# Kernel optimization log

Measured on AMD Instinct MI355X. Metric: run time of the kernel, lower is better.

Reference implementation:

```python
import jax, jax.numpy as jnp
import numpy as np

UP_RATIO = 4

def _gen_grid():
    # gen_grid(4): num_x=num_y=2, linspace(-0.2,0.2,2), meshgrid 'ij'
    g = jnp.array([-0.2, 0.2], dtype=jnp.float32)
    x, y = jnp.meshgrid(g, g, indexing='ij')
    return jnp.stack([x, y], axis=-1).reshape(-1, 2)  # [4, 2]

def setup_inputs() -> dict:
    key = jax.random.key(0)
    ks = jax.random.split(key, 12)
    B, C, N = 8, 128, 1024
    Cin = C + 2            # 130, channels after grid concat
    Cq = Cin // 4          # 32
    sc = 0.05
    f32 = jnp.float32
    inputs = jax.random.normal(ks[0], (B, C, N), f32)
    WF = jax.random.normal(ks[1], (Cq, Cin), f32) * sc
    bF = jnp.zeros((Cq,), f32)
    WG = jax.random.normal(ks[2], (Cq, Cin), f32) * sc
    bG = jnp.zeros((Cq,), f32)
    WH = jax.random.normal(ks[3], (Cin, Cin), f32) * sc
    bH = jnp.zeros((Cin,), f32)
    gamma = jnp.float32(0.5)  # torch inits to 0; nonzero so attention path is exercised
    W1 = jax.random.normal(ks[4], (256, Cin), f32) * sc
    b1 = jnp.zeros((256,), f32)
    W2 = jax.random.normal(ks[5], (128, 256), f32) * sc
    b2 = jnp.zeros((128,), f32)
    return dict(inputs=inputs, WF=WF, bF=bF, WG=WG, bG=bG, WH=WH, bH=bH,
                gamma=gamma, W1=W1, b1=b1, W2=W2, b2=b2)

def _conv1x1(W, b, x):
    # Conv1d(kernel_size=1): x [B,C,M] -> [B,O,M]
    return jnp.einsum('oc,bcm->bom', W, x) + b[:, None]

def reference(inputs, WF, bF, WG, bG, WH, bH, gamma, W1, b1, W2, b2):
    B, C, N = inputs.shape
    up = UP_RATIO
    grid = jnp.repeat(_gen_grid(), N, axis=0)          # [up*N, 2], block-repeated per grid row
    net = jnp.transpose(inputs, (0, 2, 1))             # [B, N, C]
    net = jnp.tile(net, (1, up, 1))                    # [B, up*N, C]
    net = jnp.concatenate([net, jnp.broadcast_to(grid, (B, up * N, 2))], axis=2)
    net = jnp.transpose(net, (0, 2, 1))                # [B, C+2, M]
    # attention_unit
    f = jax.nn.relu(_conv1x1(WF, bF, net))             # [B, 32, M]
    g = jax.nn.relu(_conv1x1(WG, bG, net))             # [B, 32, M]
    h = jax.nn.relu(_conv1x1(WH, bH, net))             # [B, 130, M]
    s = jnp.einsum('bcm,bcn->bmn', g, f)               # g^T f : [B, M, M]
    beta = jax.nn.softmax(s, axis=2)
    o = jnp.einsum('bck,bkm->bcm', h, beta)            # h @ beta
    x = gamma * o + net
    x = jax.nn.relu(_conv1x1(W1, b1, x))               # [B, 256, M]
    x = jax.nn.relu(_conv1x1(W2, b2, x))               # [B, 128, M]
    return x
```

## Files before the change

### kernel.cpp

```cpp
#include <hip/hip_runtime.h>
#include <hip/hip_bf16.h>
#include <math.h>

#define BB    8
#define CC    128
#define NN    1024
#define MM    4096
#define CIN   130
#define NROWS 194
#define MPAD  72
#define CIN_P 160
#define OPAD  208


typedef __attribute__((ext_vector_type(8))) short   bf16x8;
typedef __attribute__((ext_vector_type(4))) float   f32x4;
typedef __attribute__((ext_vector_type(8))) unsigned short u16x8;
typedef __attribute__((ext_vector_type(4))) unsigned short u16x4;

static __device__ __forceinline__ unsigned short f2bf(float f) {
    union { float f; unsigned u; } v; v.f = f;
    unsigned r = v.u + 0x7FFFu + ((v.u >> 16) & 1u);
    return (unsigned short)(r >> 16);
}
static __device__ __forceinline__ float bf2f(unsigned short s) {
    union { unsigned u; float f; } v; v.u = ((unsigned)s) << 16;
    return v.f;
}

#define MFMA16(a, b, c) __builtin_amdgcn_mfma_f32_16x16x32_bf16((a), (b), (c), 0, 0, 0)

__global__ __launch_bounds__(256) void prep_kernel(
    const float* __restrict__ W1, const float* __restrict__ W2,
    const float* __restrict__ WF, const float* __restrict__ WG,
    const float* __restrict__ WH, const float* __restrict__ bFp,
    const float* __restrict__ bGp, const float* __restrict__ bHp,
    unsigned short* __restrict__ W1b, unsigned short* __restrict__ W2b,
    unsigned short* __restrict__ Wfgh, float* __restrict__ bfgh,
    float* __restrict__ Lsum)
{
    int i = blockIdx.x * 256 + threadIdx.x;
    if (i < 40960) {
        int o = i / CIN_P, c = i - o * CIN_P;
        W1b[i] = (c < CIN) ? f2bf(W1[o * CIN + c]) : (unsigned short)0;
    } else if (i < 73728) {
        int j = i - 40960;
        W2b[j] = f2bf(W2[j]);
    } else if (i < 107008) {
        int j = i - 73728;
        int o = j / CIN_P, c = j - o * CIN_P;
        float w = 0.f;
        if (c < CIN) {
            if (o < 32)         w = WF[o * CIN + c];
            else if (o < 64)    w = WG[(o - 32) * CIN + c];
            else if (o < NROWS) w = WH[(o - 64) * CIN + c];
        }
        Wfgh[j] = f2bf(w);
    } else if (i < 107216) {
        int o = i - 107008;
        float bv = 0.f;
        if (o < 32)         bv = bFp[o];
        else if (o < 64)    bv = bGp[o - 32];
        else if (o < NROWS) bv = bHp[o - 64];
        bfgh[o] = bv;
    } else if (i < 139984) {
        Lsum[i - 107216] = 0.f;
    }
}

__global__ __launch_bounds__(256) void transpose_kernel(
    const float* __restrict__ inp, unsigned short* __restrict__ net_t)
{
    const int b  = blockIdx.y;
    const int n0 = blockIdx.x * 32;
    const int t  = threadIdx.x;

    __shared__ float tile[CC][33];

    for (int idx = t; idx < CC * 32; idx += 256) {
        int c = idx >> 5, n = idx & 31;
        tile[c][n] = inp[((size_t)b * CC + c) * NN + n0 + n];
    }
    __syncthreads();

    const int n = t >> 3, grp = t & 7;
    #pragma unroll
    for (int q = 0; q < 4; ++q) {
        const int m = q * NN + n0 + n;
        const float gx = (q >> 1) ? 0.2f : -0.2f;
        const float gy = (q & 1)  ? 0.2f : -0.2f;
        for (int j = grp; j < 20; j += 8) {
            const int c0 = j * 8;
            u16x8 pk;
            #pragma unroll
            for (int i = 0; i < 8; ++i) {
                int c = c0 + i;
                float v = (c < CC) ? tile[c][n]
                        : (c == CC) ? gx : (c == CC + 1) ? gy : 0.f;
                pk[i] = f2bf(v);
            }
            *(u16x8*)&net_t[((size_t)b * MM + m) * CIN_P + c0] = pk;
        }
    }
}

__global__ __launch_bounds__(256) void proj_kernel(
    const unsigned short* __restrict__ Wfgh, const float* __restrict__ bfgh,
    const unsigned short* __restrict__ net_t,
    unsigned short* __restrict__ f_t, unsigned short* __restrict__ g_t,
    unsigned short* __restrict__ h)
{
    const int lane = threadIdx.x & 63, w = threadIdx.x >> 6;
    const int l15 = lane & 15, lg = lane >> 4;
    const int mg = blockIdx.x * 64 + w * 16 + l15;
    const int b = mg >> 12, m = mg & (MM - 1);

    bf16x8 nf[5];
    #pragma unroll
    for (int ks = 0; ks < 5; ++ks)
        nf[ks] = *(const bf16x8*)&net_t[(size_t)mg * CIN_P + ks * 32 + lg * 8];

    const f32x4 zero = {0.f, 0.f, 0.f, 0.f};

    #pragma unroll
    for (int ot = 0; ot < 13; ++ot) {
        f32x4 acc = zero;
        #pragma unroll
        for (int ks = 0; ks < 5; ++ks) {
            bf16x8 aW = *(const bf16x8*)&Wfgh[(size_t)(ot * 16 + l15) * CIN_P + ks * 32 + lg * 8];
            acc = MFMA16(aW, nf[ks], acc);
        }
        const int o0 = ot * 16 + lg * 4;
        float v[4];
        #pragma unroll
        for (int r = 0; r < 4; ++r) v[r] = fmaxf(acc[r] + bfgh[o0 + r], 0.f);

        if (ot < 2) {
            u16x4 pk;
            #pragma unroll
            for (int r = 0; r < 4; ++r) pk[r] = f2bf(v[r]);
            *(u16x4*)&f_t[(size_t)mg * 32 + o0] = pk;
        } else if (ot < 4) {
            u16x4 pk;
            #pragma unroll
            for (int r = 0; r < 4; ++r) pk[r] = f2bf(v[r]);
            *(u16x4*)&g_t[(size_t)mg * 32 + (o0 - 32)] = pk;
        } else {
            #pragma unroll
            for (int r = 0; r < 4; ++r) {
                int o = o0 + r;
                if (o < NROWS)
                    h[((size_t)b * CIN + (o - 64)) * MM + m] = f2bf(v[r]);
            }
        }
    }
}

__global__ __launch_bounds__(256) void rowstats_kernel(
    const unsigned short* __restrict__ f_t, const unsigned short* __restrict__ g_t,
    float* __restrict__ Lsum)
{
    const int b  = blockIdx.y;
    const int k0 = blockIdx.x * 64;
    const int m0 = blockIdx.z * 1024;
    const int lane = threadIdx.x & 63, w = threadIdx.x >> 6;
    const int l15 = lane & 15, lg = lane >> 4;

    const bf16x8 aG = *(const bf16x8*)&g_t[((size_t)b * MM + k0 + w * 16 + l15) * 32 + lg * 8];
    const f32x4 zero = {0.f, 0.f, 0.f, 0.f};
    f32x4 sum = zero;

    for (int mc = m0; mc < m0 + 1024; mc += 64) {
        #pragma unroll
        for (int mt = 0; mt < 4; ++mt) {
            bf16x8 fB = *(const bf16x8*)&f_t[((size_t)b * MM + mc + mt * 16 + l15) * 32 + lg * 8];
            f32x4 s = MFMA16(aG, fB, zero);
            #pragma unroll
            for (int r = 0; r < 4; ++r) sum[r] += __expf(s[r] - 4.0f);
        }
    }

    #pragma unroll
    for (int d = 1; d < 16; d <<= 1) {
        #pragma unroll
        for (int r = 0; r < 4; ++r) sum[r] += __shfl_xor(sum[r], d);
    }
    if (l15 == 0) {
        #pragma unroll
        for (int r = 0; r < 4; ++r)
            atomicAdd(&Lsum[b * MM + k0 + w * 16 + lg * 4 + r], sum[r]);
    }
}

__global__ __launch_bounds__(256) void attn_kernel(
    const unsigned short* __restrict__ f_t, const unsigned short* __restrict__ g_t,
    const unsigned short* __restrict__ h,   const float* __restrict__ Lsum,
    float* __restrict__ P)
{
    const int b  = blockIdx.y;
    const int m0 = blockIdx.x * 64;
    const int kz = blockIdx.z;
    const int tid = threadIdx.x;
    const int lane = tid & 63, w = tid >> 6;
    const int l15 = lane & 15, lg = lane >> 4;

    __shared__ unsigned short Hs[144 * MPAD];
    __shared__ unsigned short Et[64 * MPAD];

    const f32x4 zero = {0.f, 0.f, 0.f, 0.f};

    bf16x8 fF[4];
    #pragma unroll
    for (int mt = 0; mt < 4; ++mt)
        fF[mt] = *(const bf16x8*)&f_t[((size_t)b * MM + m0 + mt * 16 + l15) * 32 + lg * 8];

    f32x4 acc[9];
    #pragma unroll
    for (int ct = 0; ct < 9; ++ct) acc[ct] = zero;

    const int kbeg = kz * (MM / 2), kend = kbeg + (MM / 2);
    for (int kc = kbeg; kc < kend; kc += 64) {
        bf16x8 hst[5];
        #pragma unroll
        for (int u = 0; u < 5; ++u) {
            int idx = tid + u * 256;
            int c = idx >> 3, seg = idx & 7;
            bf16x8 v = {0,0,0,0,0,0,0,0};
            if (idx < 1152 && c < CIN)
                v = *(const bf16x8*)&h[((size_t)b * CIN + c) * MM + kc + seg * 8];
            hst[u] = v;
        }

        bf16x8 aG = *(const bf16x8*)&g_t[((size_t)b * MM + kc + w * 16 + l15) * 32 + lg * 8];
        float rinv[4];
        #pragma unroll
        for (int r = 0; r < 4; ++r)
            rinv[r] = 1.0f / Lsum[b * MM + kc + w * 16 + lg * 4 + r];

        f32x4 s[4];
        #pragma unroll
        for (int mt = 0; mt < 4; ++mt)
            s[mt] = MFMA16(aG, fF[mt], zero);

        __syncthreads();

        #pragma unroll
        for (int mt = 0; mt < 4; ++mt) {
            u16x4 pk;
            #pragma unroll
            for (int r = 0; r < 4; ++r)
                pk[r] = f2bf(__expf(s[mt][r] - 4.0f) * rinv[r]);
            *(u16x4*)&Et[(size_t)(mt * 16 + l15) * MPAD + w * 16 + lg * 4] = pk;
        }
        #pragma unroll
        for (int u = 0; u < 5; ++u) {
            int idx = tid + u * 256;
            int c = idx >> 3, seg = idx & 7;
            if (idx < 1152)
                *(bf16x8*)&Hs[(size_t)c * MPAD + seg * 8] = hst[u];
        }
        __syncthreads();

        bf16x8 eB[2];
        #pragma unroll
        for (int ks = 0; ks < 2; ++ks)
            eB[ks] = *(const bf16x8*)&Et[(size_t)(w * 16 + l15) * MPAD + ks * 32 + lg * 8];
        #pragma unroll
        for (int ct = 0; ct < 9; ++ct) {
            #pragma unroll
            for (int ks = 0; ks < 2; ++ks) {
                bf16x8 aH = *(const bf16x8*)&Hs[(size_t)(ct * 16 + l15) * MPAD + ks * 32 + lg * 8];
                acc[ct] = MFMA16(aH, eB[ks], acc[ct]);
            }
        }
    }

    const int m = m0 + w * 16 + l15;
    #pragma unroll
    for (int ct = 0; ct < 9; ++ct) {
        #pragma unroll
        for (int r = 0; r < 4; ++r) {
            const int c = ct * 16 + lg * 4 + r;
            if (c < CIN)
                P[((size_t)(kz * BB + b) * CIN + c) * MM + m] = acc[ct][r];
        }
    }
}

__global__ __launch_bounds__(256) void combine_kernel(
    const float* __restrict__ P, const unsigned short* __restrict__ net_t,
    const float* __restrict__ gamma_p, unsigned short* __restrict__ x_t)
{
    const int b = blockIdx.y;
    const int moff = threadIdx.x & 63, cg = threadIdx.x >> 6;
    const int m = blockIdx.x * 64 + moff;
    const float gam = gamma_p[0];

    #pragma unroll
    for (int j = 0; j < 5; ++j) {
        const int c0 = cg * 40 + j * 8;
        u16x8 net8 = *(const u16x8*)&net_t[((size_t)b * MM + m) * CIN_P + c0];
        u16x8 pk;
        #pragma unroll
        for (int i = 0; i < 8; ++i) {
            const int c = c0 + i;
            if (c < CIN) {
                float p0 = P[((size_t)(0 * BB + b) * CIN + c) * MM + m];
                float p1 = P[((size_t)(1 * BB + b) * CIN + c) * MM + m];
                pk[i] = f2bf(gam * (p0 + p1) + bf2f(net8[i]));
            } else {
                pk[i] = 0;
            }
        }
        *(u16x8*)&x_t[((size_t)b * MM + m) * CIN_P + c0] = pk;
    }
}

template <int KS, int OT, bool OUTF32>
__global__ __launch_bounds__(256) void conv_mfma_kernel(
    const unsigned short* __restrict__ Wb, const float* __restrict__ bias,
    const unsigned short* __restrict__ in_t,
    unsigned short* __restrict__ out_bf, float* __restrict__ out_f32)
{
    const int CINP = KS * 32;
    const int lane = threadIdx.x & 63, w = threadIdx.x >> 6;
    const int l15 = lane & 15, lg = lane >> 4;
    const int m = blockIdx.x * 64 + w * 16 + l15;

    bf16x8 bFr[KS];
    #pragma unroll
    for (int ks = 0; ks < KS; ++ks)
        bFr[ks] = *(const bf16x8*)&in_t[(size_t)m * CINP + ks * 32 + lg * 8];

    const f32x4 zero = {0.f, 0.f, 0.f, 0.f};

    #pragma unroll
    for (int ot = 0; ot < OT; ++ot) {
        f32x4 acc = zero;
        #pragma unroll
        for (int ks = 0; ks < KS; ++ks) {
            bf16x8 aW = *(const bf16x8*)&Wb[(size_t)(ot * 16 + l15) * CINP + ks * 32 + lg * 8];
            acc = MFMA16(aW, bFr[ks], acc);
        }
        const int obase = ot * 16 + lg * 4;
        if (OUTF32) {
            const int bb = m >> 12, mm = m & (MM - 1);
            #pragma unroll
            for (int r = 0; r < 4; ++r)
                out_f32[((size_t)bb * (OT * 16) + obase + r) * MM + mm] =
                    fmaxf(acc[r] + bias[obase + r], 0.f);
        } else {
            u16x4 pk;
            #pragma unroll
            for (int r = 0; r < 4; ++r)
                pk[r] = f2bf(fmaxf(acc[r] + bias[obase + r], 0.f));
            *(u16x4*)&out_bf[(size_t)m * (OT * 16) + obase] = pk;
        }
    }
}

extern "C" void kernel_launch(void* const* d_in, const int* in_sizes, int n_in,
                              void* d_out, int out_size, void* d_ws, size_t ws_size,
                              hipStream_t stream)
{
    const float* inp   = (const float*)d_in[0];
    const float* WF    = (const float*)d_in[1];
    const float* bF    = (const float*)d_in[2];
    const float* WG    = (const float*)d_in[3];
    const float* bG    = (const float*)d_in[4];
    const float* WH    = (const float*)d_in[5];
    const float* bH    = (const float*)d_in[6];
    const float* gamma = (const float*)d_in[7];
    const float* W1    = (const float*)d_in[8];
    const float* b1    = (const float*)d_in[9];
    const float* W2    = (const float*)d_in[10];
    const float* b2    = (const float*)d_in[11];
    float* out = (float*)d_out;

    char* p = (char*)d_ws;
    auto alloc = [&](size_t bytes) { char* q = p; p += (bytes + 255) & ~(size_t)255; return q; };
    unsigned short* net_t = (unsigned short*)alloc((size_t)BB * MM * CIN_P * 2);
    unsigned short* f_t   = (unsigned short*)alloc((size_t)BB * MM * 32 * 2);
    unsigned short* g_t   = (unsigned short*)alloc((size_t)BB * MM * 32 * 2);
    unsigned short* h     = (unsigned short*)alloc((size_t)BB * CIN * MM * 2);
    float*          Lsum  = (float*)alloc((size_t)BB * MM * 4);
    unsigned short* x_t   = (unsigned short*)alloc((size_t)BB * MM * CIN_P * 2);
    float*          P     = (float*)alloc((size_t)2 * BB * CIN * MM * 4);
    unsigned short* x1_t  = (unsigned short*)P;
    unsigned short* W1b   = (unsigned short*)alloc((size_t)256 * CIN_P * 2);
    unsigned short* W2b   = (unsigned short*)alloc((size_t)128 * 256 * 2);
    unsigned short* Wfgh  = (unsigned short*)alloc((size_t)OPAD * CIN_P * 2);
    float*          bfgh  = (float*)alloc((size_t)OPAD * 4);

    prep_kernel<<<547, 256, 0, stream>>>(W1, W2, WF, WG, WH, bF, bG, bH,
                                         W1b, W2b, Wfgh, bfgh, Lsum);

    transpose_kernel<<<dim3(NN / 32, BB), 256, 0, stream>>>(inp, net_t);

    proj_kernel<<<dim3(BB * MM / 64), 256, 0, stream>>>(
        Wfgh, bfgh, net_t, f_t, g_t, h);

    rowstats_kernel<<<dim3(MM / 64, BB, 4), 256, 0, stream>>>(f_t, g_t, Lsum);

    attn_kernel<<<dim3(MM / 64, BB, 2), 256, 0, stream>>>(f_t, g_t, h, Lsum, P);

    combine_kernel<<<dim3(MM / 64, BB), 256, 0, stream>>>(P, net_t, gamma, x_t);

    conv_mfma_kernel<5, 16, false><<<dim3(BB * MM / 64), 256, 0, stream>>>(
        W1b, b1, x_t, x1_t, nullptr);

    conv_mfma_kernel<8, 8, true><<<dim3(BB * MM / 64), 256, 0, stream>>>(
        W2b, b2, x1_t, nullptr, out);
}
```

Baseline: 298.3 us.

## Restructure attention kernel into per-wave 32-column tiles with direct global H loads

The attention kernel now processes 128 output columns per block, with each wave owning 32 columns and computing its own 64-key score tile into a private, XOR-swizzled LDS region. The shared H staging and the block-wide __syncthreads are removed: H fragments are read directly from global memory and reused across two column tiles. The reciprocal is switched to a hardware rcp. The aim is to drop block barriers and LDS traffic for H, at the cost of redundant global H reads per wave, recomputation of exp per wave, and halving the grid size.

After: 372.4 us. 1.25x slower.

```diff
diff --git a/kernel.cpp b/kernel.cpp
--- a/kernel.cpp
+++ b/kernel.cpp
@@ -8,7 +8,6 @@
 #define MM    4096
 #define CIN   130
 #define NROWS 194
-#define MPAD  72
 #define CIN_P 160
 #define OPAD  208
 
@@ -198,91 +197,91 @@
     float* __restrict__ P)
 {
     const int b  = blockIdx.y;
-    const int m0 = blockIdx.x * 64;
+    const int m0 = blockIdx.x * 128;
     const int kz = blockIdx.z;
     const int tid = threadIdx.x;
     const int lane = tid & 63, w = tid >> 6;
     const int l15 = lane & 15, lg = lane >> 4;
 
-    __shared__ unsigned short Hs[144 * MPAD];
-    __shared__ unsigned short Et[64 * MPAD];
+    __shared__ unsigned short Et[4 * 2048];
+    unsigned short* et = &Et[w * 2048];
+    const int swzx = (l15 & 7) << 3;
 
     const f32x4 zero = {0.f, 0.f, 0.f, 0.f};
 
-    bf16x8 fF[4];
-    #pragma unroll
-    for (int mt = 0; mt < 4; ++mt)
-        fF[mt] = *(const bf16x8*)&f_t[((size_t)b * MM + m0 + mt * 16 + l15) * 32 + lg * 8];
-
-    f32x4 acc[9];
-    #pragma unroll
-    for (int ct = 0; ct < 9; ++ct) acc[ct] = zero;
+    bf16x8 fF[2];
+    #pragma unroll
+    for (int mt = 0; mt < 2; ++mt)
+        fF[mt] = *(const bf16x8*)&f_t[((size_t)b * MM + m0 + w * 32 + mt * 16 + l15) * 32 + lg * 8];
+
+    f32x4 acc[9][2];
+    #pragma unroll
+    for (int ct = 0; ct < 9; ++ct)
+        #pragma unroll
+        for (int mt = 0; mt < 2; ++mt) acc[ct][mt] = zero;
 
     const int kbeg = kz * (MM / 2), kend = kbeg + (MM / 2);
     for (int kc = kbeg; kc < kend; kc += 64) {
-        bf16x8 hst[5];
-        #pragma unroll
-        for (int u = 0; u < 5; ++u) {
-            int idx = tid + u * 256;
-            int c = idx >> 3, seg = idx & 7;
-            bf16x8 v = {0,0,0,0,0,0,0,0};
-            if (idx < 1152 && c < CIN)
-                v = *(const bf16x8*)&h[((size_t)b * CIN + c) * MM + kc + seg * 8];
-            hst[u] = v;
-        }
-
-        bf16x8 aG = *(const bf16x8*)&g_t[((size_t)b * MM + kc + w * 16 + l15) * 32 + lg * 8];
-        float rinv[4];
-        #pragma unroll
-        for (int r = 0; r < 4; ++r)
-            rinv[r] = 1.0f / Lsum[b * MM + kc + w * 16 + lg * 4 + r];
-
-        f32x4 s[4];
-        #pragma unroll
-        for (int mt = 0; mt < 4; ++mt)
-            s[mt] = MFMA16(aG, fF[mt], zero);
-
-        __syncthreads();
-
-        #pragma unroll
-        for (int mt = 0; mt < 4; ++mt) {
-            u16x4 pk;
-            #pragma unroll
-            for (int r = 0; r < 4; ++r)
-                pk[r] = f2bf(__expf(s[mt][r] - 4.0f) * rinv[r]);
-            *(u16x4*)&Et[(size_t)(mt * 16 + l15) * MPAD + w * 16 + lg * 4] = pk;
-        }
-        #pragma unroll
-        for (int u = 0; u < 5; ++u) {
-            int idx = tid + u * 256;
-            int c = idx >> 3, seg = idx & 7;
-            if (idx < 1152)
-                *(bf16x8*)&Hs[(size_t)c * MPAD + seg * 8] = hst[u];
-        }
-        __syncthreads();
-
-        bf16x8 eB[2];
-        #pragma unroll
-        for (int ks = 0; ks < 2; ++ks)
-            eB[ks] = *(const bf16x8*)&Et[(size_t)(w * 16 + l15) * MPAD + ks * 32 + lg * 8];
+        bf16x8 aG[4];
+        #pragma unroll
+        for (int kt = 0; kt < 4; ++kt)
+            aG[kt] = *(const bf16x8*)&g_t[((size_t)b * MM + kc + kt * 16 + l15) * 32 + lg * 8];
+        f32x4 rv[4];
+        #pragma unroll
+        for (int kt = 0; kt < 4; ++kt) {
+            f32x4 ls = *(const f32x4*)&Lsum[b * MM + kc + kt * 16 + lg * 4];
+            #pragma unroll
+            for (int r = 0; r < 4; ++r) rv[kt][r] = __builtin_amdgcn_rcpf(ls[r]);
+        }
+        #pragma unroll
+        for (int mt = 0; mt < 2; ++mt) {
+            #pragma unroll
+            for (int kt = 0; kt < 4; ++kt) {
+                f32x4 s = MFMA16(aG[kt], fF[mt], zero);
+                u16x4 pk;
+                #pragma unroll
+                for (int r = 0; r < 4; ++r)
+                    pk[r] = f2bf(__expf(s[r] - 4.0f) * rv[kt][r]);
+                *(u16x4*)&et[(mt * 16 + l15) * 64 + ((kt * 16 + lg * 4) ^ swzx)] = pk;
+            }
+        }
+
+        asm volatile("s_waitcnt lgkmcnt(0)" ::: "memory");
+        __builtin_amdgcn_sched_barrier(0);
+
+        bf16x8 eB[2][2];
+        #pragma unroll
+        for (int mt = 0; mt < 2; ++mt)
+            #pragma unroll
+            for (int ks = 0; ks < 2; ++ks)
+                eB[mt][ks] = *(const bf16x8*)&et[(mt * 16 + l15) * 64 + ((ks * 32 + lg * 8) ^ swzx)];
+
         #pragma unroll
         for (int ct = 0; ct < 9; ++ct) {
+            const int c = ct * 16 + l15;
             #pragma unroll
             for (int ks = 0; ks < 2; ++ks) {
-                bf16x8 aH = *(const bf16x8*)&Hs[(size_t)(ct * 16 + l15) * MPAD + ks * 32 + lg * 8];
-                acc[ct] = MFMA16(aH, eB[ks], acc[ct]);
-            }
-        }
-    }
-
-    const int m = m0 + w * 16 + l15;
+                bf16x8 aH = {0,0,0,0,0,0,0,0};
+                if (c < CIN)
+                    aH = *(const bf16x8*)&h[((size_t)b * CIN + c) * MM + kc + ks * 32 + lg * 8];
+                #pragma unroll
+                for (int mt = 0; mt < 2; ++mt)
+                    acc[ct][mt] = MFMA16(aH, eB[mt][ks], acc[ct][mt]);
+            }
+        }
+    }
+
     #pragma unroll
     for (int ct = 0; ct < 9; ++ct) {
         #pragma unroll
-        for (int r = 0; r < 4; ++r) {
-            const int c = ct * 16 + lg * 4 + r;
-            if (c < CIN)
-                P[((size_t)(kz * BB + b) * CIN + c) * MM + m] = acc[ct][r];
+        for (int mt = 0; mt < 2; ++mt) {
+            const int m = m0 + w * 32 + mt * 16 + l15;
+            #pragma unroll
+            for (int r = 0; r < 4; ++r) {
+                const int c = ct * 16 + lg * 4 + r;
+                if (c < CIN)
+                    P[((size_t)(kz * BB + b) * CIN + c) * MM + m] = acc[ct][mt][r];
+            }
         }
     }
 }
@@ -402,7 +401,7 @@
 
     rowstats_kernel<<<dim3(MM / 64, BB, 4), 256, 0, stream>>>(f_t, g_t, Lsum);
 
-    attn_kernel<<<dim3(MM / 64, BB, 2), 256, 0, stream>>>(f_t, g_t, h, Lsum, P);
+    attn_kernel<<<dim3(MM / 128, BB, 2), 256, 0, stream>>>(f_t, g_t, h, Lsum, P);
 
     combine_kernel<<<dim3(MM / 64, BB), 256, 0, stream>>>(P, net_t, gamma, x_t);
 
```
